# Performance work log

Measured on AMD Instinct MI355X. Metric: run time of the kernel, lower is better.

Reference implementation:

```python
import jax, jax.numpy as jnp
import numpy as np

V, D, MAXLEN, B, C = 32000, 1024, 2048, 4, 2048


def setup_inputs() -> dict:
    key = jax.random.key(0)
    ks = jax.random.split(key, 8)
    x = jax.random.randint(ks[0], (B, C), 0, V, dtype=jnp.int64)
    s = 0.02
    embed = jax.random.normal(ks[1], (V, D), dtype=jnp.float32) * s
    pe = jax.random.normal(ks[2], (MAXLEN, D), dtype=jnp.float32) * s
    Wq = jax.random.normal(ks[3], (D, D), dtype=jnp.float32) * s
    Wk = jax.random.normal(ks[4], (D, D), dtype=jnp.float32) * s
    Wv = jax.random.normal(ks[5], (D, D), dtype=jnp.float32) * s
    Wo = jax.random.normal(ks[6], (V, D), dtype=jnp.float32) * s
    bo = jnp.zeros((V,), dtype=jnp.float32)
    return {"x": x, "embed": embed, "pe": pe, "Wq": Wq, "Wk": Wk, "Wv": Wv, "Wo": Wo, "bo": bo}


def reference(x, embed, pe, Wq, Wk, Wv, Wo, bo):
    Bc, Cc = x.shape
    Dd = embed.shape[1]
    # token embedding + learned absolute PE (pos_offset = 0)
    h = embed[x] + pe[:Cc]                      # (B, C, D)
    # single-head Q/K/V projections (torch Linear: y = x @ W.T)
    Q = jnp.einsum('bcd,ed->bce', h, Wq)
    K = jnp.einsum('bcd,ed->bce', h, Wk)
    Vv = jnp.einsum('bcd,ed->bce', h, Wv)
    scores = jnp.einsum('bqd,bkd->bqk', Q, K) / jnp.sqrt(jnp.float32(Dd))
    # additive causal mask: 0 on lower triangle, -inf above
    mask = jnp.where(jnp.tril(jnp.ones((Cc, Cc), dtype=bool)), 0.0, -jnp.inf).astype(scores.dtype)
    weights = jax.nn.softmax(scores + mask, axis=-1)  # (B, C, C)
    attn_out = jnp.einsum('bqk,bkd->bqd', weights, Vv)
    hidden = h + attn_out
    logits = jnp.einsum('bcd,vd->bcv', hidden, Wo) + bo
    return logits
```

## Files before the change

kernel.cpp:

```cpp
#include <hip/hip_runtime.h>

#define DEV __device__ __forceinline__

typedef __attribute__((ext_vector_type(8))) __bf16 bf16x8;
typedef __attribute__((ext_vector_type(4))) float f32x4;

DEV unsigned short f2bf(float f) {
    unsigned u = __builtin_bit_cast(unsigned, f);
    u += 0x7fffu + ((u >> 16) & 1u);
    return (unsigned short)(u >> 16);
}
DEV float bf2f(unsigned short s) {
    unsigned u = ((unsigned)s) << 16;
    return __builtin_bit_cast(float, u);
}

DEV void gload_lds16(const unsigned short* g, unsigned short* l) {
    __builtin_amdgcn_global_load_lds(
        (const __attribute__((address_space(1))) unsigned int*)g,
        (__attribute__((address_space(3))) unsigned int*)l, 16, 0, 0);
}


__global__ __launch_bounds__(256) void k_cast_bf16(const float* __restrict__ src,
                                                   unsigned short* __restrict__ dst, int n4) {
    int i = blockIdx.x * 256 + threadIdx.x;
    if (i >= n4) return;
    float4 v = reinterpret_cast<const float4*>(src)[i];
    ushort4 o;
    o.x = f2bf(v.x); o.y = f2bf(v.y); o.z = f2bf(v.z); o.w = f2bf(v.w);
    reinterpret_cast<ushort4*>(dst)[i] = o;
}

__global__ __launch_bounds__(256) void k_cast3(const float* __restrict__ a,
                                               const float* __restrict__ b,
                                               const float* __restrict__ c,
                                               unsigned short* __restrict__ oa,
                                               unsigned short* __restrict__ ob,
                                               unsigned short* __restrict__ oc,
                                               int n4each) {
    int i = blockIdx.x * 256 + threadIdx.x;
    int w = i / n4each, j = i - w * n4each;
    const float* s = (w == 0) ? a : (w == 1) ? b : c;
    unsigned short* d = (w == 0) ? oa : (w == 1) ? ob : oc;
    float4 v = reinterpret_cast<const float4*>(s)[j];
    ushort4 o;
    o.x = f2bf(v.x); o.y = f2bf(v.y); o.z = f2bf(v.z); o.w = f2bf(v.w);
    reinterpret_cast<ushort4*>(d)[j] = o;
}

__global__ __launch_bounds__(256) void k_prep_h(const int* __restrict__ x,
                                                const float* __restrict__ embed,
                                                const float* __restrict__ pe,
                                                unsigned short* __restrict__ h) {
    const int r = blockIdx.x;
    const int pos = r & 2047;
    const int tok = x[r];
    const int t = threadIdx.x;
    float4 e = reinterpret_cast<const float4*>(embed + (size_t)tok * 1024)[t];
    float4 p = reinterpret_cast<const float4*>(pe + (size_t)pos * 1024)[t];
    ushort4 o;
    o.x = f2bf(e.x + p.x); o.y = f2bf(e.y + p.y);
    o.z = f2bf(e.z + p.z); o.w = f2bf(e.w + p.w);
    reinterpret_cast<ushort4*>(h + (size_t)r * 1024)[t] = o;
}

__global__ __launch_bounds__(256) void k_softmax_causal(const float* __restrict__ S,
                                                        unsigned short* __restrict__ W) {
    const int r = blockIdx.x;
    const int q = r & 2047;
    const float* row = S + (size_t)r * 2048;
    unsigned short* orow = W + (size_t)r * 2048;
    const int t = threadIdx.x;
    const float scale = 0.03125f;
    const int kceil4 = (((q >> 7) + 1) << 7) >> 2;
    float p[8];
    float mx = -1e30f;
    #pragma unroll
    for (int i = 0; i < 2; ++i) {
        int i4 = t + i * 256;
        int base = i4 * 4;
        float4 v = (float4){0.f, 0.f, 0.f, 0.f};
        if (base <= q) v = reinterpret_cast<const float4*>(row)[i4];
        p[i*4+0] = (base+0 <= q) ? v.x * scale : -1e30f;
        p[i*4+1] = (base+1 <= q) ? v.y * scale : -1e30f;
        p[i*4+2] = (base+2 <= q) ? v.z * scale : -1e30f;
        p[i*4+3] = (base+3 <= q) ? v.w * scale : -1e30f;
        #pragma unroll
        for (int j = 0; j < 4; ++j) mx = fmaxf(mx, p[i*4+j]);
    }
    #pragma unroll
    for (int o = 32; o > 0; o >>= 1) mx = fmaxf(mx, __shfl_xor(mx, o));
    __shared__ float redm[4];
    __shared__ float reds[4];
    const int w = t >> 6;
    if ((t & 63) == 0) redm[w] = mx;
    __syncthreads();
    mx = fmaxf(fmaxf(redm[0], redm[1]), fmaxf(redm[2], redm[3]));
    float e[8];
    float s = 0.f;
    #pragma unroll
    for (int i = 0; i < 8; ++i) { e[i] = __expf(p[i] - mx); s += e[i]; }
    #pragma unroll
    for (int o = 32; o > 0; o >>= 1) s += __shfl_xor(s, o);
    if ((t & 63) == 0) reds[w] = s;
    __syncthreads();
    s = (reds[0] + reds[1]) + (reds[2] + reds[3]);
    const float inv = 1.0f / s;
    #pragma unroll
    for (int i = 0; i < 2; ++i) {
        int i4 = t + i * 256;
        if (i4 < kceil4) {
            ushort4 o4;
            o4.x = f2bf(e[i*4+0] * inv);
            o4.y = f2bf(e[i*4+1] * inv);
            o4.z = f2bf(e[i*4+2] * inv);
            o4.w = f2bf(e[i*4+3] * inv);
            reinterpret_cast<ushort4*>(orow)[i4] = o4;
        }
    }
}

template<int OUT_BF16, int TRANS_OUT, int ADD_BIAS, int ADD_RES, int CAUSAL_SKIP, int TRI_K>
__global__ __launch_bounds__(256)
void k_gemm_bt(const unsigned short* __restrict__ A,
               const unsigned short* __restrict__ B,
               void* __restrict__ Out,
               const float* __restrict__ bias,
               const unsigned short* __restrict__ Res,
               int M, int N, int K, int ldo,
               long long sA, long long sB, long long sC, long long sRes) {
    const int bm = blockIdx.x, bn = blockIdx.y, bz = blockIdx.z;
    if (CAUSAL_SKIP && bn > bm) return;
    A += (long long)bz * sA;
    B += (long long)bz * sB;

    __shared__ __align__(16) unsigned short As[128 * 32];
    __shared__ __align__(16) unsigned short Bs[128 * 32];

    const int t = threadIdx.x;
    const int w = t >> 6;
    const int lane = t & 63;
    const int wm = w >> 1, wn = w & 1;
    const int fr = lane & 15, fq = lane >> 4;

    f32x4 acc[4][4];
    #pragma unroll
    for (int mi = 0; mi < 4; ++mi)
        #pragma unroll
        for (int ni = 0; ni < 4; ++ni)
            acc[mi][ni] = (f32x4){0.f, 0.f, 0.f, 0.f};

    const int kend = TRI_K ? ((K < (bm + 1) * 128) ? K : (bm + 1) * 128) : K;

    const int c0 = t, c1 = t + 256;
    const unsigned short* gA0 = A + (size_t)(bm * 128 + (c0 >> 2)) * K + (c0 & 3) * 8;
    const unsigned short* gA1 = A + (size_t)(bm * 128 + (c1 >> 2)) * K + (c1 & 3) * 8;
    const unsigned short* gB0 = B + (size_t)(bn * 128 + (c0 >> 2)) * K + (c0 & 3) * 8;
    const unsigned short* gB1 = B + (size_t)(bn * 128 + (c1 >> 2)) * K + (c1 & 3) * 8;
    unsigned short* lA0 = As + w * 512;
    unsigned short* lA1 = As + 2048 + w * 512;
    unsigned short* lB0 = Bs + w * 512;
    unsigned short* lB1 = Bs + 2048 + w * 512;

    for (int kt = 0; kt < kend; kt += 32) {
        gload_lds16(gA0 + kt, lA0);
        gload_lds16(gA1 + kt, lA1);
        gload_lds16(gB0 + kt, lB0);
        gload_lds16(gB1 + kt, lB1);
        __syncthreads();

        bf16x8 af[4], bfr[4];
        #pragma unroll
        for (int mi = 0; mi < 4; ++mi)
            af[mi] = *reinterpret_cast<const bf16x8*>(As + (wm * 64 + mi * 16 + fr) * 32 + fq * 8);
        #pragma unroll
        for (int ni = 0; ni < 4; ++ni)
            bfr[ni] = *reinterpret_cast<const bf16x8*>(Bs + (wn * 64 + ni * 16 + fr) * 32 + fq * 8);
        #pragma unroll
        for (int mi = 0; mi < 4; ++mi)
            #pragma unroll
            for (int ni = 0; ni < 4; ++ni)
                acc[mi][ni] = __builtin_amdgcn_mfma_f32_16x16x32_bf16(af[mi], bfr[ni], acc[mi][ni], 0, 0, 0);
        __syncthreads();
    }

    const int row0 = bm * 128 + wm * 64 + fq * 4;
    const int col0 = bn * 128 + wn * 64 + fr;
    if (OUT_BF16) {
        unsigned short* O = (unsigned short*)Out + (long long)bz * sC;
        #pragma unroll
        for (int mi = 0; mi < 4; ++mi) {
            #pragma unroll
            for (int j = 0; j < 4; ++j) {
                const int row = row0 + mi * 16 + j;
                unsigned short* orow = O + (size_t)row * ldo;
                const unsigned short* rrow =
                    ADD_RES ? (Res + (long long)bz * sRes + (size_t)row * ldo) : (const unsigned short*)nullptr;
                #pragma unroll
                for (int ni = 0; ni < 4; ++ni) {
                    const int col = col0 + ni * 16;
                    float v = acc[mi][ni][j];
                    if (ADD_RES) v += bf2f(rrow[col]);
                    orow[col] = f2bf(v);
                }
            }
        }
    } else {
        float* O = (float*)Out + (long long)bz * sC;
        #pragma unroll
        for (int mi = 0; mi < 4; ++mi) {
            #pragma unroll
            for (int j = 0; j < 4; ++j) {
                const int row = row0 + mi * 16 + j;
                float* orow = O + (size_t)row * ldo;
                #pragma unroll
                for (int ni = 0; ni < 4; ++ni) {
                    const int col = col0 + ni * 16;
                    float v = acc[mi][ni][j];
                    if (ADD_BIAS) v += bias[col];
                    orow[col] = v;
                }
            }
        }
    }
}


#define SA3(buf, kt) do { \
    unsigned short* d_ = Lds + (buf)*16384 + w*512; \
    gload_lds16(gA0 + (kt)*32, d_); \
    gload_lds16(gA1 + (kt)*32, d_ + 4096); } while(0)

#define SB3(buf, kt) do { \
    unsigned short* d_ = Lds + (buf)*16384 + 8192 + w*512; \
    gload_lds16(gB0 + (kt)*32, d_); \
    gload_lds16(gB1 + (kt)*32, d_ + 4096); } while(0)

#define LDA3(buf, mi) (*reinterpret_cast<const bf16x8*>(Lds + (buf)*16384 + aBase + (mi)*512))
#define LDB3(buf, ni) (*reinterpret_cast<const bf16x8*>(Lds + (buf)*16384 + 8192 + bBase + (ni)*512))

#define MF16(arow, af) do { \
    __builtin_amdgcn_s_setprio(1); \
    _Pragma("unroll") \
    for (int j_ = 0; j_ < 4; ++j_) \
        _Pragma("unroll") \
        for (int n_ = 0; n_ < 4; ++n_) \
            acc[(arow)+j_][n_] = __builtin_amdgcn_mfma_f32_16x16x32_bf16(af[j_], bb[n_], acc[(arow)+j_][n_], 0, 0, 0); \
    __builtin_amdgcn_s_setprio(0); } while(0)

#define BARX asm volatile("s_barrier" ::: "memory")

template<int EPI>
__global__ __launch_bounds__(512, 2)
void k_g256(const unsigned short* __restrict__ A,
            const unsigned short* __restrict__ B,
            void* __restrict__ O0, void* __restrict__ O1, void* __restrict__ O2,
            const float* __restrict__ bias) {
    constexpr int K = 1024;
    __shared__ __align__(16) unsigned short Lds[65536];

    int bm, bn, bz = 0;
    if (EPI == 2) {
        bm = blockIdx.x; bn = blockIdx.y; bz = blockIdx.z;
        if (bn > bm) return;
    } else if (EPI == 1) {
        int wg = blockIdx.x;
        wg = (wg & 7) * 48 + (wg >> 3);
        bm = wg % 32; bn = wg / 32;
    } else {
        int wg = blockIdx.x;
        wg = (wg & 7) * 500 + (wg >> 3);
        const int tb = wg / 20, u = wg % 20;
        bm = (tb & 7) * 4 + (u & 3);
        bn = (tb >> 3) * 5 + (u >> 2);
    }

    const unsigned short* Ab = A + (EPI == 2 ? (size_t)bz * 2048 * K : 0);
    const unsigned short* Bb2 = B + (EPI == 2 ? (size_t)bz * 2048 * K : 0);

    const int tid = threadIdx.x;
    const int w = tid >> 6, lane = tid & 63;
    const int wm = w >> 2, wn = w & 3;
    const int fr = lane & 15, fq = lane >> 4;
    const int sl = fq ^ ((fr >> 1) & 3);

    const int c0 = w * 64 + lane, c1 = c0 + 512;
    const int r0 = c0 >> 2, s0 = ((c0 & 3) ^ ((r0 >> 1) & 3)) * 8;
    const int r1 = c1 >> 2, s1 = ((c1 & 3) ^ ((r1 >> 1) & 3)) * 8;
    const unsigned short* gA0 = Ab + (size_t)(bm * 256 + r0) * K + s0;
    const unsigned short* gA1 = Ab + (size_t)(bm * 256 + r1) * K + s1;
    const unsigned short* gB0 = Bb2 + (size_t)(bn * 256 + r0) * K + s0;
    const unsigned short* gB1 = Bb2 + (size_t)(bn * 256 + r1) * K + s1;

    const int aBase = (wm * 128 + fr) * 32 + sl * 8;
    const int bBase = (wn * 64 + fr) * 32 + sl * 8;

    f32x4 acc[8][4];
    #pragma unroll
    for (int i = 0; i < 8; ++i)
        #pragma unroll
        for (int j = 0; j < 4; ++j)
            acc[i][j] = (f32x4){0.f, 0.f, 0.f, 0.f};

    SA3(0, 0); SB3(0, 0);
    SA3(1, 1); SB3(1, 1);
    SA3(2, 2); SB3(2, 2);
    asm volatile("s_waitcnt vmcnt(8)" ::: "memory");
    BARX;
    bf16x8 a0[4], bb[4];
    #pragma unroll
    for (int j = 0; j < 4; ++j) a0[j] = LDA3(0, j);
    #pragma unroll
    for (int j = 0; j < 4; ++j) bb[j] = LDB3(0, j);

    #pragma unroll
    for (int t = 0; t < 32; ++t) {
        const int bc = t & 3, b1 = (t + 1) & 3, bs = (t + 3) & 3;
        const int ks = (t + 3) & 31;
        bf16x8 a1t[4];
        #pragma unroll
        for (int j = 0; j < 4; ++j) a1t[j] = LDA3(bc, 4 + j);
        SA3(bs, ks);
        BARX;
        MF16(0, a0);
        asm volatile("s_waitcnt vmcnt(6)" ::: "memory");
        BARX;
        bf16x8 a0n[4], bn_[4];
        #pragma unroll
        for (int j = 0; j < 4; ++j) a0n[j] = LDA3(b1, j);
        #pragma unroll
        for (int j = 0; j < 4; ++j) bn_[j] = LDB3(b1, j);
        SB3(bs, ks);
        BARX;
        MF16(4, a1t);
        BARX;
        #pragma unroll
        for (int j = 0; j < 4; ++j) { a0[j] = a0n[j]; bb[j] = bn_[j]; }
    }
    asm volatile("s_waitcnt vmcnt(0)" ::: "memory");

    const int row0 = bm * 256 + wm * 128 + fq * 4;
    const int col0 = bn * 256 + wn * 64 + fr;
    if (EPI == 0) {
        float* Out = (float*)O0;
        float bia[4];
        #pragma unroll
        for (int ni = 0; ni < 4; ++ni) bia[ni] = bias[col0 + ni * 16];
        #pragma unroll
        for (int mi = 0; mi < 8; ++mi) {
            #pragma unroll
            for (int j = 0; j < 4; ++j) {
                float* orow = Out + (size_t)(row0 + mi * 16 + j) * 32000;
                #pragma unroll
                for (int ni = 0; ni < 4; ++ni)
                    orow[col0 + ni * 16] = acc[mi][ni][j] + bia[ni];
            }
        }
    } else if (EPI == 1) {
        if (bn < 8) {
            unsigned short* O = (unsigned short*)(bn < 4 ? O0 : O1);
            const int cb = (bn < 4) ? 0 : 1024;
            #pragma unroll
            for (int mi = 0; mi < 8; ++mi) {
                #pragma unroll
                for (int j = 0; j < 4; ++j) {
                    unsigned short* orow = O + (size_t)(row0 + mi * 16 + j) * 1024;
                    #pragma unroll
                    for (int ni = 0; ni < 4; ++ni)
                        orow[col0 + ni * 16 - cb] = f2bf(acc[mi][ni][j]);
                }
            }
        } else {
            unsigned short* O = (unsigned short*)O2 + (size_t)(row0 >> 11) * 2097152;
            const int i0 = row0 & 2047;
            #pragma unroll
            for (int mi = 0; mi < 8; ++mi) {
                #pragma unroll
                for (int ni = 0; ni < 4; ++ni) {
                    const int e = col0 + ni * 16 - 2048;
                    ushort4 o4;
                    o4.x = f2bf(acc[mi][ni][0]);
                    o4.y = f2bf(acc[mi][ni][1]);
                    o4.z = f2bf(acc[mi][ni][2]);
                    o4.w = f2bf(acc[mi][ni][3]);
                    *reinterpret_cast<ushort4*>(O + (size_t)e * 2048 + i0 + mi * 16) = o4;
                }
            }
        }
    } else {
        float* Out = (float*)O0 + (size_t)bz * 2048 * 2048;
        #pragma unroll
        for (int mi = 0; mi < 8; ++mi) {
            #pragma unroll
            for (int j = 0; j < 4; ++j) {
                float* orow = Out + (size_t)(row0 + mi * 16 + j) * 2048;
                #pragma unroll
                for (int ni = 0; ni < 4; ++ni)
                    orow[col0 + ni * 16] = acc[mi][ni][j];
            }
        }
    }
}


extern "C" void kernel_launch(void* const* d_in, const int* in_sizes, int n_in,
                              void* d_out, int out_size, void* d_ws, size_t ws_size,
                              hipStream_t stream) {
    (void)in_sizes; (void)n_in; (void)out_size; (void)ws_size;
    constexpr int Bb = 4, Cc = 2048, Dd = 1024, Vv = 32000;
    constexpr int M = Bb * Cc;

    const int*   x     = (const int*)d_in[0];
    const float* embed = (const float*)d_in[1];
    const float* pe    = (const float*)d_in[2];
    const float* Wq    = (const float*)d_in[3];
    const float* Wk    = (const float*)d_in[4];
    const float* Wv    = (const float*)d_in[5];
    const float* Wo    = (const float*)d_in[6];
    const float* bo    = (const float*)d_in[7];
    float* out = (float*)d_out;

    char* p = (char*)d_ws;
    auto au = [&](size_t n) { unsigned short* r = (unsigned short*)p; p += n * sizeof(unsigned short); return r; };
    unsigned short* h_bf   = au((size_t)M * Dd);
    unsigned short* hid_bf = au((size_t)M * Dd);
    unsigned short* Qb     = au((size_t)M * Dd);
    unsigned short* Kb     = au((size_t)M * Dd);
    unsigned short* Vt     = au((size_t)M * Dd);
    unsigned short* Wqb    = au((size_t)Dd * Dd);
    unsigned short* Wkb    = au((size_t)Dd * Dd);
    unsigned short* Wvb    = au((size_t)Dd * Dd);
    unsigned short* Wob    = au((size_t)Vv * Dd);
    unsigned short* Wt     = au((size_t)Bb * Cc * Cc);
    float* Sc = (float*)p;

    k_cast3<<<dim3(3 * Dd * Dd / 4 / 256), 256, 0, stream>>>(Wq, Wk, Wv, Wqb, Wkb, Wvb, Dd * Dd / 4);
    k_cast_bf16<<<dim3(Vv * Dd / 4 / 256), 256, 0, stream>>>(Wo, Wob, Vv * Dd / 4);
    k_prep_h<<<dim3(M), 256, 0, stream>>>(x, embed, pe, h_bf);

    k_g256<1><<<dim3(384), 512, 0, stream>>>(h_bf, Wqb, Qb, Kb, Vt, nullptr);

    k_g256<2><<<dim3(8, 8, 4), 512, 0, stream>>>(Qb, Kb, Sc, nullptr, nullptr, nullptr);

    k_softmax_causal<<<dim3(M), 256, 0, stream>>>(Sc, Wt);

    {
        dim3 g(Cc / 128, Dd / 128, Bb);
        k_gemm_bt<1,0,0,1,0,1><<<g, 256, 0, stream>>>(Wt, Vt, hid_bf, nullptr, h_bf,
            Cc, Dd, Cc, Dd, (long long)Cc * Cc, (long long)Dd * Cc, (long long)Cc * Dd, (long long)Cc * Dd);
    }

    k_g256<0><<<dim3(4000), 512, 0, stream>>>(hid_bf, Wob, out, nullptr, nullptr, bo);
}
```

Measured before the change: 800.2 us.

## Use a 4-stage LDS pipeline kernel for the output-logits GEMM

Moves the logits GEMM (hidden × Wo) out of the shared templated kernel into a dedicated kernel. The new kernel keeps a four-buffer LDS ring with three K-slices prefetched ahead and a single barrier per K step, instead of the multi-barrier split main loop. The aim is to overlap global-to-LDS loads with MFMA work and cut barrier stalls in the largest GEMM. In exchange it depends on the SA3/SB3 buffer indexing supporting four stages within the LDS size, and the deeper prefetch may change register pressure.

```diff
diff --git a/kernel.cpp b/kernel.cpp
--- a/kernel.cpp
+++ b/kernel.cpp
@@ -264,16 +264,10 @@
     if (EPI == 2) {
         bm = blockIdx.x; bn = blockIdx.y; bz = blockIdx.z;
         if (bn > bm) return;
-    } else if (EPI == 1) {
+    } else {
         int wg = blockIdx.x;
         wg = (wg & 7) * 48 + (wg >> 3);
         bm = wg % 32; bn = wg / 32;
-    } else {
-        int wg = blockIdx.x;
-        wg = (wg & 7) * 500 + (wg >> 3);
-        const int tb = wg / 20, u = wg % 20;
-        bm = (tb & 7) * 4 + (u & 3);
-        bn = (tb >> 3) * 5 + (u >> 2);
     }
 
     const unsigned short* Ab = A + (EPI == 2 ? (size_t)bz * 2048 * K : 0);
@@ -342,22 +336,7 @@
 
     const int row0 = bm * 256 + wm * 128 + fq * 4;
     const int col0 = bn * 256 + wn * 64 + fr;
-    if (EPI == 0) {
-        float* Out = (float*)O0;
-        float bia[4];
-        #pragma unroll
-        for (int ni = 0; ni < 4; ++ni) bia[ni] = bias[col0 + ni * 16];
-        #pragma unroll
-        for (int mi = 0; mi < 8; ++mi) {
-            #pragma unroll
-            for (int j = 0; j < 4; ++j) {
-                float* orow = Out + (size_t)(row0 + mi * 16 + j) * 32000;
-                #pragma unroll
-                for (int ni = 0; ni < 4; ++ni)
-                    orow[col0 + ni * 16] = acc[mi][ni][j] + bia[ni];
-            }
-        }
-    } else if (EPI == 1) {
+    if (EPI == 1) {
         if (bn < 8) {
             unsigned short* O = (unsigned short*)(bn < 4 ? O0 : O1);
             const int cb = (bn < 4) ? 0 : 1024;
@@ -404,6 +383,92 @@
 }
 
 
+__global__ __launch_bounds__(512, 2)
+void k_glog2(const unsigned short* __restrict__ A,
+             const unsigned short* __restrict__ B,
+             float* __restrict__ Out,
+             const float* __restrict__ bias) {
+    constexpr int K = 1024;
+    __shared__ __align__(16) unsigned short Lds[65536];
+
+    int wg = blockIdx.x;
+    wg = (wg & 7) * 500 + (wg >> 3);
+    const int tb = wg / 20, u = wg % 20;
+    const int bm = (tb & 7) * 4 + (u & 3);
+    const int bn = (tb >> 3) * 5 + (u >> 2);
+
+    const int tid = threadIdx.x;
+    const int w = tid >> 6, lane = tid & 63;
+    const int wm = w >> 2, wn = w & 3;
+    const int fr = lane & 15, fq = lane >> 4;
+    const int sl = fq ^ ((fr >> 1) & 3);
+
+    const int c0 = w * 64 + lane, c1 = c0 + 512;
+    const int r0 = c0 >> 2, s0 = ((c0 & 3) ^ ((r0 >> 1) & 3)) * 8;
+    const int r1 = c1 >> 2, s1 = ((c1 & 3) ^ ((r1 >> 1) & 3)) * 8;
+    const unsigned short* gA0 = A + (size_t)(bm * 256 + r0) * K + s0;
+    const unsigned short* gA1 = A + (size_t)(bm * 256 + r1) * K + s1;
+    const unsigned short* gB0 = B + (size_t)(bn * 256 + r0) * K + s0;
+    const unsigned short* gB1 = B + (size_t)(bn * 256 + r1) * K + s1;
+
+    const int aBase = (wm * 128 + fr) * 32 + sl * 8;
+    const int bBase = (wn * 64 + fr) * 32 + sl * 8;
+
+    f32x4 acc[8][4];
+    #pragma unroll
+    for (int i = 0; i < 8; ++i)
+        #pragma unroll
+        for (int j = 0; j < 4; ++j)
+            acc[i][j] = (f32x4){0.f, 0.f, 0.f, 0.f};
+
+    SA3(0, 0); SB3(0, 0);
+    SA3(1, 1); SB3(1, 1);
+    SA3(2, 2); SB3(2, 2);
+    asm volatile("s_waitcnt vmcnt(8)" ::: "memory");
+    BARX;
+
+    #pragma unroll
+    for (int t = 0; t < 32; ++t) {
+        const int bc = t & 3, bs = (t + 3) & 3;
+        const int ks = (t + 3) & 31;
+        SA3(bs, ks);
+        SB3(bs, ks);
+        bf16x8 af[8], bf_[4];
+        #pragma unroll
+        for (int mi = 0; mi < 8; ++mi) af[mi] = LDA3(bc, mi);
+        #pragma unroll
+        for (int ni = 0; ni < 4; ++ni) bf_[ni] = LDB3(bc, ni);
+        __builtin_amdgcn_s_setprio(1);
+        #pragma unroll
+        for (int mi = 0; mi < 8; ++mi)
+            #pragma unroll
+            for (int ni = 0; ni < 4; ++ni)
+                acc[mi][ni] = __builtin_amdgcn_mfma_f32_16x16x32_bf16(af[mi], bf_[ni], acc[mi][ni], 0, 0, 0);
+        __builtin_amdgcn_s_setprio(0);
+        asm volatile("s_waitcnt vmcnt(8)" ::: "memory");
+        BARX;
+    }
+    asm volatile("s_waitcnt vmcnt(0)" ::: "memory");
+
+    const int row0 = bm * 256 + wm * 128 + fq * 4;
+    const int col0 = bn * 256 + wn * 64 + fr;
+    float bia[4];
+    #pragma unroll
+    for (int ni = 0; ni < 4; ++ni) bia[ni] = bias[col0 + ni * 16];
+    #pragma unroll
+    for (int mi = 0; mi < 8; ++mi) {
+        #pragma unroll
+        for (int j = 0; j < 4; ++j) {
+            float* orow = Out + (size_t)(row0 + mi * 16 + j) * 32000;
+            #pragma unroll
+            for (int ni = 0; ni < 4; ++ni)
+                orow[col0 + ni * 16] = acc[mi][ni][j] + bia[ni];
+        }
+    }
+    asm volatile("s_waitcnt vmcnt(0)" ::: "memory");
+}
+
+
 extern "C" void kernel_launch(void* const* d_in, const int* in_sizes, int n_in,
                               void* d_out, int out_size, void* d_ws, size_t ws_size,
                               hipStream_t stream) {
@@ -451,5 +516,5 @@
             Cc, Dd, Cc, Dd, (long long)Cc * Cc, (long long)Dd * Cc, (long long)Cc * Dd, (long long)Cc * Dd);
     }
 
-    k_g256<0><<<dim3(4000), 512, 0, stream>>>(hid_bf, Wob, out, nullptr, nullptr, bo);
-}
+    k_glog2<<<dim3(4000), 512, 0, stream>>>(hid_bf, Wob, out, bo);
+}
```

New measurement: 801.6 us. Within noise of the previous version (+0.2%).
